# Performance work log

Measured on AMD Instinct MI355X. Metric: run time of the kernel, lower is better.

The kernel has to match this reference:

```python
import math
import jax, jax.numpy as jnp
import numpy as np

EMB = 1024
NHEADS = 16
CTX = 2048
LN_EPS = 1e-5


def new_gelu(x):
    c = math.sqrt(2.0 / math.pi)
    return 0.5 * x * (1.0 + jnp.tanh(c * (x + 0.044715 * x * x * x)))


def layer_norm(x, g, b):
    mu = jnp.mean(x, axis=-1, keepdims=True)
    var = jnp.mean(jnp.square(x - mu), axis=-1, keepdims=True)
    return (x - mu) * jax.lax.rsqrt(var + LN_EPS) * g + b


def setup_inputs() -> dict:
    key = jax.random.key(0)
    ks = jax.random.split(key, 12)
    s = 0.02
    return {
        "x": jax.random.normal(ks[0], (2, 2048, EMB), dtype=jnp.float32),
        "ln1_g": jnp.ones((EMB,), jnp.float32),
        "ln1_b": jnp.zeros((EMB,), jnp.float32),
        "W_attn": jax.random.normal(ks[1], (EMB, 3 * EMB), jnp.float32) * s,
        "b_attn": jnp.zeros((3 * EMB,), jnp.float32),
        "W_attn_proj": jax.random.normal(ks[2], (EMB, EMB), jnp.float32) * s,
        "b_attn_proj": jnp.zeros((EMB,), jnp.float32),
        "ln2_g": jnp.ones((EMB,), jnp.float32),
        "ln2_b": jnp.zeros((EMB,), jnp.float32),
        "W_fc": jax.random.normal(ks[3], (EMB, 4 * EMB), jnp.float32) * s,
        "b_fc": jnp.zeros((4 * EMB,), jnp.float32),
        "W_mlp_proj": jax.random.normal(ks[4], (4 * EMB, EMB), jnp.float32) * s,
        "b_mlp_proj": jnp.zeros((EMB,), jnp.float32),
    }


def reference(x, ln1_g, ln1_b, W_attn, b_attn, W_attn_proj, b_attn_proj,
              ln2_g, ln2_b, W_fc, b_fc, W_mlp_proj, b_mlp_proj):
    B, S, E = x.shape
    hd = E // NHEADS

    # x = ln_1(x)
    x = layer_norm(x, ln1_g, ln1_b)

    # attention on normalized x
    qkv = x @ W_attn + b_attn                      # [B,S,3E]
    q, k, v = jnp.split(qkv, 3, axis=-1)
    q = q.reshape(B, S, NHEADS, hd).transpose(0, 2, 1, 3)  # [B,H,S,hd]
    k = k.reshape(B, S, NHEADS, hd).transpose(0, 2, 1, 3)
    v = v.reshape(B, S, NHEADS, hd).transpose(0, 2, 1, 3)

    attn = jnp.einsum("bhqd,bhkd->bhqk", q, k) * (1.0 / math.sqrt(hd))
    causal = jnp.tril(jnp.ones((S, S), dtype=bool))
    attn = jnp.where(causal[None, None], attn, -jnp.inf)
    attn = jax.nn.softmax(attn, axis=-1)
    out = jnp.einsum("bhqk,bhkd->bhqd", attn, v)   # [B,H,S,hd]
    out = out.transpose(0, 2, 1, 3).reshape(B, S, E)
    out = out @ W_attn_proj + b_attn_proj

    x = x + out

    # x = ln_2(x)
    x = layer_norm(x, ln2_g, ln2_b)

    # MLP on normalized x
    h = new_gelu(x @ W_fc + b_fc)
    h = h @ W_mlp_proj + b_mlp_proj
    return x + h
```

## Files before the change

kernel.cpp:

```cpp
#include <hip/hip_runtime.h>
#include <cstdint>

typedef __attribute__((ext_vector_type(8))) short bf16x8;
typedef __attribute__((ext_vector_type(4))) float f32x4;
typedef __attribute__((ext_vector_type(16))) float f32x16;
typedef __attribute__((ext_vector_type(4))) unsigned short u16x4;
typedef __attribute__((ext_vector_type(4))) unsigned int u32x4;
typedef unsigned short u16;

#define LOG2E 1.44269504088896340736f

__device__ __forceinline__ u16 f2bf(float f) {
  unsigned u = __builtin_bit_cast(unsigned, f);
  u += 0x7FFFu + ((u >> 16) & 1u);
  return (u16)(u >> 16);
}
__device__ __forceinline__ float bf2f(u16 h) {
  return __builtin_bit_cast(float, ((unsigned)h) << 16);
}

#define GLOAD_LDS16(g, l)                                                              \
  __builtin_amdgcn_global_load_lds((const __attribute__((address_space(1))) void*)(g), \
                                   (__attribute__((address_space(3))) void*)(l), 16, 0, 0)

__global__ __launch_bounds__(256) void k_transpose_all(
    const float* __restrict__ W0, u16* __restrict__ T0,
    const float* __restrict__ W1, u16* __restrict__ T1,
    const float* __restrict__ W2, u16* __restrict__ T2,
    const float* __restrict__ W3, u16* __restrict__ T3) {
  __shared__ float tile[32][33];
  int b = blockIdx.x;
  const float* W;
  u16* Wt;
  int K, N, nx;
  if (b < 3072)        { W = W0; Wt = T0; K = 1024; N = 3072; nx = 96; }
  else if (b < 4096)   { b -= 3072; W = W1; Wt = T1; K = 1024; N = 1024; nx = 32; }
  else if (b < 8192)   { b -= 4096; W = W2; Wt = T2; K = 1024; N = 4096; nx = 128; }
  else                 { b -= 8192; W = W3; Wt = T3; K = 4096; N = 1024; nx = 32; }
  const int n0 = (b % nx) * 32, k0 = (b / nx) * 32;
  const int tid = threadIdx.x;
  const int tx = tid & 31, ty = tid >> 5;
#pragma unroll
  for (int i = 0; i < 32; i += 8)
    tile[ty + i][tx] = W[(size_t)(k0 + ty + i) * N + n0 + tx];
  __syncthreads();
#pragma unroll
  for (int i = 0; i < 32; i += 8)
    Wt[(size_t)(n0 + ty + i) * K + k0 + tx] = f2bf(tile[tx][ty + i]);
}

template <bool INF32>
__global__ __launch_bounds__(256) void k_layernorm(
    const void* __restrict__ xin, const float* __restrict__ g,
    const float* __restrict__ b, u16* __restrict__ y) {
  const int row = blockIdx.x, tid = threadIdx.x;
  float v0, v1, v2, v3;
  if (INF32) {
    const float4 v = ((const float4*)((const float*)xin + (size_t)row * 1024))[tid];
    v0 = v.x; v1 = v.y; v2 = v.z; v3 = v.w;
  } else {
    const u16x4 v = ((const u16x4*)((const u16*)xin + (size_t)row * 1024))[tid];
    v0 = bf2f(v[0]); v1 = bf2f(v[1]); v2 = bf2f(v[2]); v3 = bf2f(v[3]);
  }
  float s = v0 + v1 + v2 + v3;
#pragma unroll
  for (int m = 1; m < 64; m <<= 1) s += __shfl_xor(s, m);
  __shared__ float ps[8];
  if ((tid & 63) == 0) ps[tid >> 6] = s;
  __syncthreads();
  const float mean = (ps[0] + ps[1] + ps[2] + ps[3]) * (1.0f / 1024.0f);
  const float d0 = v0 - mean, d1 = v1 - mean, d2 = v2 - mean, d3 = v3 - mean;
  float s2 = d0 * d0 + d1 * d1 + d2 * d2 + d3 * d3;
#pragma unroll
  for (int m = 1; m < 64; m <<= 1) s2 += __shfl_xor(s2, m);
  if ((tid & 63) == 0) ps[4 + (tid >> 6)] = s2;
  __syncthreads();
  const float var = (ps[4] + ps[5] + ps[6] + ps[7]) * (1.0f / 1024.0f);
  const float rstd = rsqrtf(var + 1e-5f);
  const float4 gv = ((const float4*)g)[tid];
  const float4 bv = ((const float4*)b)[tid];
  u16x4 o;
  o[0] = f2bf(d0 * rstd * gv.x + bv.x);
  o[1] = f2bf(d1 * rstd * gv.y + bv.y);
  o[2] = f2bf(d2 * rstd * gv.z + bv.z);
  o[3] = f2bf(d3 * rstd * gv.w + bv.w);
  *(u16x4*)(y + (size_t)row * 1024 + tid * 4) = o;
}

__device__ __forceinline__ float gelu_f(float x) {
  const float u = 0.7978845608028654f * (x + 0.044715f * x * x * x);
  const float e = exp2f(u * 2.8853900817779268f);
  const float t = 1.0f - 2.0f / (e + 1.0f);
  return 0.5f * x * (1.0f + t);
}

template <int EPI, int BN>
__global__ __launch_bounds__(256, 4) void k_gemm_bt(
    const u16* __restrict__ A, const u16* __restrict__ Bt,
    const float* __restrict__ bias, const u16* __restrict__ resid,
    void* __restrict__ out, u16* __restrict__ vt, int M, int N, int K, int nbx) {
  constexpr int BM = 128;
  constexpr int LOOPB = (BM * 64 + BN * 64) * 2;
  constexpr int STP = BN + 8;
  constexpr int EPIB = (EPI == 1) ? 64 * 68 * 4 : BM * STP * 2;
  constexpr int SMB = LOOPB > EPIB ? LOOPB : EPIB;
  __shared__ char smem[SMB];
  u16* As = (u16*)smem;
  u16* Bs = (u16*)(smem + BM * 64 * 2);
  const int tid = threadIdx.x;
  const int wg = ((blockIdx.x & 7) * (gridDim.x >> 3)) + (blockIdx.x >> 3);
  const int bx = wg % nbx, by = wg / nbx;
  const int rowBase = by * BM, colBase = bx * BN;
  const int w = tid >> 6, l = tid & 63;
  const int wm = (BN == 128) ? (w >> 1) : w;
  const int wn = (BN == 128) ? (w & 1) : 0;
  constexpr int MR = (BN == 128) ? 4 : 2;
  constexpr int WROWS = (BN == 128) ? 64 : 32;
  const int lrow = l & 15, lg = l >> 4;
  const int srow = tid >> 3, sslot = tid & 7;

  const f32x4 fz = {0.f, 0.f, 0.f, 0.f};
  f32x4 acc[MR][4];
#pragma unroll
  for (int m = 0; m < MR; m++)
#pragma unroll
    for (int n = 0; n < 4; n++) acc[m][n] = fz;

  const int NT = K >> 6;
  for (int kt = 0; kt < NT; ++kt) {
#pragma unroll
    for (int i = 0; i < BM / 32; i++) {
      const int r = srow + 32 * i;
      const int gs = sslot ^ (r & 7);
      GLOAD_LDS16(A + (size_t)(rowBase + r) * K + kt * 64 + gs * 8,
                  (char*)As + i * 4096 + tid * 16);
    }
#pragma unroll
    for (int i = 0; i < BN / 32; i++) {
      const int r = srow + 32 * i;
      const int gs = sslot ^ (r & 7);
      GLOAD_LDS16(Bt + (size_t)(colBase + r) * K + kt * 64 + gs * 8,
                  (char*)Bs + i * 4096 + tid * 16);
    }
    __syncthreads();
#pragma unroll
    for (int kc = 0; kc < 2; kc++) {
      bf16x8 av[MR], bv[4];
#pragma unroll
      for (int m = 0; m < MR; m++) {
        const int r = wm * WROWS + m * 16 + lrow;
        const int sl = (kc * 4 + lg) ^ (r & 7);
        av[m] = *(const bf16x8*)((const char*)As + r * 128 + sl * 16);
      }
#pragma unroll
      for (int n = 0; n < 4; n++) {
        const int r = wn * 64 + n * 16 + lrow;
        const int sl = (kc * 4 + lg) ^ (r & 7);
        bv[n] = *(const bf16x8*)((const char*)Bs + r * 128 + sl * 16);
      }
#pragma unroll
      for (int m = 0; m < MR; m++)
#pragma unroll
        for (int n = 0; n < 4; n++)
          acc[m][n] = __builtin_amdgcn_mfma_f32_16x16x32_bf16(av[m], bv[n], acc[m][n], 0, 0, 0);
    }
    __syncthreads();
  }

  if (EPI == 1) {
    float* stgf = (float*)smem;
#pragma unroll
    for (int m = 0; m < MR; m++) {
      if (m) __syncthreads();
#pragma unroll
      for (int n = 0; n < 4; n++) {
        const int col = n * 16 + lrow;
        const float bval = bias[colBase + col];
        const int pr0 = wm * 16 + lg * 4;
#pragma unroll
        for (int r = 0; r < 4; r++) stgf[(pr0 + r) * 68 + col] = acc[m][n][r] + bval;
      }
      __syncthreads();
#pragma unroll
      for (int i = 0; i < 4; i++) {
        const int c = i * 256 + tid;
        const int pr = c >> 4, ch = c & 15;
        float4 d = *(float4*)(stgf + pr * 68 + ch * 4);
        const int grow = rowBase + ((pr >> 4) << 5) + m * 16 + (pr & 15);
        const size_t gidx = (size_t)grow * N + colBase + ch * 4;
        const u16x4 rr = *(const u16x4*)(resid + gidx);
        d.x += bf2f(rr[0]); d.y += bf2f(rr[1]); d.z += bf2f(rr[2]); d.w += bf2f(rr[3]);
        *(float4*)((float*)out + gidx) = d;
      }
    }
  } else {
    u16* stg = (u16*)smem;
    const bool vpath = (EPI == 3) && (colBase >= 2048);
#pragma unroll
    for (int n = 0; n < 4; n++) {
      const int col = wn * 64 + n * 16 + lrow;
      const float bval = bias[colBase + col];
#pragma unroll
      for (int m = 0; m < MR; m++) {
        const int lr0 = wm * WROWS + m * 16 + lg * 4;
#pragma unroll
        for (int r = 0; r < 4; r++) {
          float v = acc[m][n][r] + bval;
          if (EPI == 2) v = gelu_f(v);
          if (vpath)
            stg[col * STP + lr0 + r] = f2bf(v);
          else
            stg[(lr0 + r) * STP + col] = f2bf(v);
        }
      }
    }
    __syncthreads();
    if (vpath) {
      const int cb = colBase - 2048;
      const int bat = rowBase >> 11, tok0 = rowBase & 2047;
#pragma unroll
      for (int i = 0; i < 8; i++) {
        const int c = i * 256 + tid;
        const int cr = c >> 4, ch = c & 15;
        const u32x4 d = *(u32x4*)(stg + cr * STP + ch * 8);
        const int hh = (cb + cr) >> 6, dd = (cb + cr) & 63;
        *(u32x4*)(vt + ((size_t)(bat * 16 + hh) * 64 + dd) * 2048 + tok0 + ch * 8) = d;
      }
    } else {
      const int outN = (EPI == 3) ? 2048 : N;
      constexpr int CH = BN / 8;
#pragma unroll
      for (int i = 0; i < BM * CH / 256; i++) {
        const int c = i * 256 + tid;
        const int row = c / CH, ch = c % CH;
        u32x4 d = *(u32x4*)(stg + row * STP + ch * 8);
        const size_t gidx = (size_t)(rowBase + row) * outN + colBase + ch * 8;
        if (EPI == 4) {
          const u32x4 rr = *(const u32x4*)(resid + gidx);
#pragma unroll
          for (int j = 0; j < 4; j++) {
            const unsigned a = d[j], b = rr[j];
            const unsigned lo2 = (unsigned)f2bf(bf2f((u16)a) + bf2f((u16)b));
            const unsigned hi2 = (unsigned)f2bf(bf2f((u16)(a >> 16)) + bf2f((u16)(b >> 16)));
            d[j] = lo2 | (hi2 << 16);
          }
        }
        *(u32x4*)((u16*)out + gidx) = d;
      }
    }
  }
}

__global__ __launch_bounds__(256, 2) void k_attention(
    const u16* __restrict__ qk, const u16* __restrict__ VT, u16* __restrict__ out) {
  const int S = 2048, E2 = 2048;
  const int bid = blockIdx.x;
  const int qt = 15 - (bid >> 5);
  const int bh = bid & 31;
  const int bat = bh >> 4, h = bh & 15;
  const u16* base = qk + (size_t)bat * S * E2;
  const u16* kbase = base + 1024 + h * 64;
  const u16* vbase = VT + (size_t)bh * 64 * S;
  const int tid = threadIdx.x, w = tid >> 6, l = tid & 63;
  const int l31 = l & 31, lh = l >> 5;
  __shared__ u16 Ks[2][128 * 64];
  __shared__ u16 Vs[2][64 * 128];
  const int ksrow = tid >> 3;
  const int kgs = (tid & 7) ^ (ksrow & 7);
  const int vsrow = tid >> 4;
  const int vgs = (tid & 15) ^ (vsrow & 15);
  const float sc = 0.125f * LOG2E;
  const float RTHR = 8.0f / sc;

  auto STAGE = [&](int bufi, int kb) {
#pragma unroll
    for (int i = 0; i < 4; i++) {
      const int kr = ksrow + 32 * i;
      GLOAD_LDS16(kbase + (size_t)(kb + kr) * E2 + kgs * 8,
                  (char*)Ks[bufi] + i * 4096 + tid * 16);
      const int vr = vsrow + 16 * i;
      GLOAD_LDS16(vbase + (size_t)vr * S + kb + vgs * 8,
                  (char*)Vs[bufi] + i * 4096 + tid * 16);
    }
  };

  const int wq0 = qt * 128 + w * 32;
  const int qg = wq0 + l31;
  const int nkt = qt + 1;

  bf16x8 qf[4];
#pragma unroll
  for (int s = 0; s < 4; s++)
    qf[s] = *(const bf16x8*)(base + (size_t)qg * E2 + h * 64 + s * 16 + lh * 8);

  f32x16 o0, o1;
#pragma unroll
  for (int r = 0; r < 16; r++) { o0[r] = 0.f; o1[r] = 0.f; }
  float mrow = -1e30f, lsum = 0.f;

  STAGE(0, 0);
  __syncthreads();

  for (int t = 0; t < nkt; t++) {
    const int cur = t & 1;
    const int kb = t * 128;
    if (t + 1 < nkt) STAGE(cur ^ 1, kb + 128);
    const u16* Kc = Ks[cur];
    const u16* Vc = Vs[cur];

    f32x16 sv[4];
#pragma unroll
    for (int j = 0; j < 4; j++)
#pragma unroll
      for (int r = 0; r < 16; r++) sv[j][r] = 0.f;
#pragma unroll
    for (int s = 0; s < 4; s++) {
      const int sl = s * 2 + lh;
#pragma unroll
      for (int j = 0; j < 4; j++) {
        const int rk = j * 32 + l31;
        const bf16x8 kf = *(const bf16x8*)(Kc + rk * 64 + ((sl ^ (rk & 7)) * 8));
        sv[j] = __builtin_amdgcn_mfma_f32_32x32x16_bf16(kf, qf[s], sv[j], 0, 0, 0);
      }
    }

    if (t == nkt - 1) {
#pragma unroll
      for (int j = 0; j < 4; j++)
#pragma unroll
        for (int reg = 0; reg < 16; reg++) {
          const int kl = (reg & 3) + 8 * (reg >> 2) + 4 * lh;
          if (kb + j * 32 + kl > qg) sv[j][reg] = -1e30f;
        }
    }

    float tmax = sv[0][0];
#pragma unroll
    for (int j = 0; j < 4; j++)
#pragma unroll
      for (int reg = 0; reg < 16; reg++) tmax = fmaxf(tmax, sv[j][reg]);
    tmax = fmaxf(tmax, __shfl_xor(tmax, 32));

    if (!__all(tmax - mrow <= RTHR)) {
      const float mnew = fmaxf(mrow, tmax);
      const float corr = exp2f((mrow - mnew) * sc);
      lsum *= corr;
#pragma unroll
      for (int reg = 0; reg < 16; reg++) { o0[reg] *= corr; o1[reg] *= corr; }
      mrow = mnew;
    }
    const float msc = mrow * sc;

    float rsum = 0.f;
#pragma unroll
    for (int j = 0; j < 4; j++)
#pragma unroll
      for (int reg = 0; reg < 16; reg++) {
        const float p = exp2f(fmaf(sv[j][reg], sc, -msc));
        sv[j][reg] = p;
        rsum += p;
      }
    rsum += __shfl_xor(rsum, 32);
    lsum += rsum;

    const bool lo = (lh == 0);
#pragma unroll
    for (int j = 0; j < 4; j++) {
      unsigned pk[8], ex[8];
#pragma unroll
      for (int jj = 0; jj < 8; jj++) {
        asm("v_cvt_pk_bf16_f32 %0, %1, %2"
            : "=v"(pk[jj])
            : "v"(sv[j][2 * jj]), "v"(sv[j][2 * jj + 1]));
        ex[jj] = (unsigned)__shfl_xor((int)pk[jj], 32);
      }
#pragma unroll
      for (int sl2 = 0; sl2 < 2; sl2++) {
        const int ks = j * 2 + sl2;
        const int j0 = sl2 * 4;
        const unsigned b0 = lo ? pk[j0 + 0] : ex[j0 + 2];
        const unsigned b1 = lo ? pk[j0 + 1] : ex[j0 + 3];
        const unsigned b2 = lo ? ex[j0 + 0] : pk[j0 + 2];
        const unsigned b3 = lo ? ex[j0 + 1] : pk[j0 + 3];
        const u32x4 pbu = {b0, b1, b2, b3};
        const bf16x8 pb = __builtin_bit_cast(bf16x8, pbu);
        const int svl = ks * 2 + lh;
        const int r0 = l31, r1 = 32 + l31;
        const bf16x8 v0 = *(const bf16x8*)(Vc + r0 * 128 + ((svl ^ (r0 & 15)) * 8));
        const bf16x8 v1 = *(const bf16x8*)(Vc + r1 * 128 + ((svl ^ (r1 & 15)) * 8));
        o0 = __builtin_amdgcn_mfma_f32_32x32x16_bf16(v0, pb, o0, 0, 0, 0);
        o1 = __builtin_amdgcn_mfma_f32_32x32x16_bf16(v1, pb, o1, 0, 0, 0);
      }
    }
    __syncthreads();
  }

  const float inv = 1.0f / lsum;
  const size_t orow = (size_t)(bat * S + qg) * 1024 + h * 64;
#pragma unroll
  for (int g = 0; g < 4; g++) {
    u16x4 s0, s1;
#pragma unroll
    for (int r = 0; r < 4; r++) {
      s0[r] = f2bf(o0[4 * g + r] * inv);
      s1[r] = f2bf(o1[4 * g + r] * inv);
    }
    const int d0 = 8 * g + 4 * lh;
    *(u16x4*)(out + orow + d0) = s0;
    *(u16x4*)(out + orow + 32 + d0) = s1;
  }
}

extern "C" void kernel_launch(void* const* d_in, const int* in_sizes, int n_in,
                              void* d_out, int out_size, void* d_ws, size_t ws_size,
                              hipStream_t stream) {
  (void)in_sizes; (void)n_in; (void)out_size; (void)ws_size;
  const float* x      = (const float*)d_in[0];
  const float* ln1_g  = (const float*)d_in[1];
  const float* ln1_b  = (const float*)d_in[2];
  const float* W_attn = (const float*)d_in[3];
  const float* b_attn = (const float*)d_in[4];
  const float* W_proj = (const float*)d_in[5];
  const float* b_proj = (const float*)d_in[6];
  const float* ln2_g  = (const float*)d_in[7];
  const float* ln2_b  = (const float*)d_in[8];
  const float* W_fc   = (const float*)d_in[9];
  const float* b_fc   = (const float*)d_in[10];
  const float* W_mlp  = (const float*)d_in[11];
  const float* b_mlp  = (const float*)d_in[12];

  const int M = 4096;
  char* ws = (char*)d_ws;
  size_t off = 0;
  auto alloc = [&](size_t bytes) {
    void* p = ws + off;
    off += (bytes + 255) & ~(size_t)255;
    return p;
  };
  u16* WattnT = (u16*)alloc((size_t)3072 * 1024 * 2);
  u16* WprojT = (u16*)alloc((size_t)1024 * 1024 * 2);
  u16* WfcT   = (u16*)alloc((size_t)4096 * 1024 * 2);
  u16* WmlpT  = (u16*)alloc((size_t)1024 * 4096 * 2);
  u16* x1     = (u16*)alloc((size_t)M * 1024 * 2);
  u16* qkb    = (u16*)alloc((size_t)M * 2048 * 2);
  u16* VT     = (u16*)alloc((size_t)32 * 64 * 2048 * 2);
  u16* attno  = (u16*)alloc((size_t)M * 1024 * 2);
  u16* x2     = (u16*)alloc((size_t)M * 1024 * 2);
  u16* x3     = (u16*)alloc((size_t)M * 1024 * 2);
  u16* hbuf   = (u16*)alloc((size_t)M * 4096 * 2);

  const dim3 blk(256);
  k_transpose_all<<<dim3(12288), blk, 0, stream>>>(
      W_attn, WattnT, W_proj, WprojT, W_fc, WfcT, W_mlp, WmlpT);

  k_layernorm<true><<<M, blk, 0, stream>>>(x, ln1_g, ln1_b, x1);
  k_gemm_bt<3, 128><<<dim3(768), blk, 0, stream>>>(
      x1, WattnT, b_attn, nullptr, qkb, VT, M, 3072, 1024, 24);
  k_attention<<<dim3(512), blk, 0, stream>>>(qkb, VT, attno);
  k_gemm_bt<4, 64><<<dim3(512), blk, 0, stream>>>(
      attno, WprojT, b_proj, x1, x2, nullptr, M, 1024, 1024, 16);
  k_layernorm<false><<<M, blk, 0, stream>>>(x2, ln2_g, ln2_b, x3);
  k_gemm_bt<2, 128><<<dim3(1024), blk, 0, stream>>>(
      x3, WfcT, b_fc, nullptr, hbuf, nullptr, M, 4096, 1024, 32);
  k_gemm_bt<1, 64><<<dim3(512), blk, 0, stream>>>(
      hbuf, WmlpT, b_mlp, x3, d_out, nullptr, M, 1024, 4096, 16);
}
```

Measured before the change: 235.8 us.

## Split long causal attention query tiles across two key ranges and combine

Query tiles 8-15, which carry the longest causal key ranges, are each split into two blocks that cover halves of the key range. Each half writes unnormalized fp32 partial outputs plus its row max and sum to workspace, and a new combine kernel merges them with log-sum-exp weights. The grid grows from 512 to 768 blocks, which evens out per-block work and cuts the long tail on the causal triangle. The cost is an extra kernel launch and fp32 partial-output traffic.

```diff
diff --git a/kernel.cpp b/kernel.cpp
--- a/kernel.cpp
+++ b/kernel.cpp
@@ -252,11 +252,20 @@
 }
 
 __global__ __launch_bounds__(256, 2) void k_attention(
-    const u16* __restrict__ qk, const u16* __restrict__ VT, u16* __restrict__ out) {
+    const u16* __restrict__ qk, const u16* __restrict__ VT, u16* __restrict__ out,
+    float* __restrict__ Op0, float* __restrict__ Op1,
+    float2* __restrict__ ml0, float2* __restrict__ ml1) {
   const int S = 2048, E2 = 2048;
   const int bid = blockIdx.x;
-  const int qt = 15 - (bid >> 5);
-  const int bh = bid & 31;
+  const int u = bid >> 5, bh = bid & 31;
+  int qt, piece;
+  if (u < 8)       { qt = 15 - u;      piece = 0; }
+  else if (u < 16) { qt = 15 - (u - 8); piece = 1; }
+  else             { qt = 23 - u;      piece = 2; }
+  const int nkt = qt + 1;
+  const int h0 = (nkt + 1) >> 1;
+  const int t0 = (piece == 1) ? h0 : 0;
+  const int t1 = (piece == 0) ? h0 : nkt;
   const int bat = bh >> 4, h = bh & 15;
   const u16* base = qk + (size_t)bat * S * E2;
   const u16* kbase = base + 1024 + h * 64;
@@ -286,7 +295,6 @@
 
   const int wq0 = qt * 128 + w * 32;
   const int qg = wq0 + l31;
-  const int nkt = qt + 1;
 
   bf16x8 qf[4];
 #pragma unroll
@@ -298,13 +306,13 @@
   for (int r = 0; r < 16; r++) { o0[r] = 0.f; o1[r] = 0.f; }
   float mrow = -1e30f, lsum = 0.f;
 
-  STAGE(0, 0);
+  STAGE(0, t0 * 128);
   __syncthreads();
 
-  for (int t = 0; t < nkt; t++) {
-    const int cur = t & 1;
+  for (int t = t0; t < t1; t++) {
+    const int cur = (t - t0) & 1;
     const int kb = t * 128;
-    if (t + 1 < nkt) STAGE(cur ^ 1, kb + 128);
+    if (t + 1 < t1) STAGE(cur ^ 1, kb + 128);
     const u16* Kc = Ks[cur];
     const u16* Vc = Vs[cur];
 
@@ -395,20 +403,57 @@
     __syncthreads();
   }
 
-  const float inv = 1.0f / lsum;
-  const size_t orow = (size_t)(bat * S + qg) * 1024 + h * 64;
-#pragma unroll
-  for (int g = 0; g < 4; g++) {
-    u16x4 s0, s1;
-#pragma unroll
-    for (int r = 0; r < 4; r++) {
-      s0[r] = f2bf(o0[4 * g + r] * inv);
-      s1[r] = f2bf(o1[4 * g + r] * inv);
-    }
-    const int d0 = 8 * g + 4 * lh;
-    *(u16x4*)(out + orow + d0) = s0;
-    *(u16x4*)(out + orow + 32 + d0) = s1;
+  if (piece == 2) {
+    const float inv = 1.0f / lsum;
+    const size_t orow = (size_t)(bat * S + qg) * 1024 + h * 64;
+#pragma unroll
+    for (int g = 0; g < 4; g++) {
+      u16x4 s0, s1;
+#pragma unroll
+      for (int r = 0; r < 4; r++) {
+        s0[r] = f2bf(o0[4 * g + r] * inv);
+        s1[r] = f2bf(o1[4 * g + r] * inv);
+      }
+      const int d0 = 8 * g + 4 * lh;
+      *(u16x4*)(out + orow + d0) = s0;
+      *(u16x4*)(out + orow + 32 + d0) = s1;
+    }
+  } else {
+    float* Op = piece ? Op1 : Op0;
+    float2* mlp = piece ? ml1 : ml0;
+    const size_t rix = (size_t)bh * 1024 + (qg - 1024);
+    const size_t rbase = rix * 64;
+#pragma unroll
+    for (int g = 0; g < 4; g++) {
+      const int d0 = 8 * g + 4 * lh;
+      float4 a, b;
+      a.x = o0[4 * g]; a.y = o0[4 * g + 1]; a.z = o0[4 * g + 2]; a.w = o0[4 * g + 3];
+      b.x = o1[4 * g]; b.y = o1[4 * g + 1]; b.z = o1[4 * g + 2]; b.w = o1[4 * g + 3];
+      *(float4*)(Op + rbase + d0) = a;
+      *(float4*)(Op + rbase + 32 + d0) = b;
+    }
+    if (lh == 0) mlp[rix] = make_float2(mrow, lsum);
   }
+}
+
+__global__ __launch_bounds__(256) void k_attn_combine(
+    const float* __restrict__ Op0, const float* __restrict__ Op1,
+    const float2* __restrict__ ml0, const float2* __restrict__ ml1,
+    u16* __restrict__ out) {
+  const float sc = 0.125f * LOG2E;
+  const int idx = blockIdx.x * 256 + threadIdx.x;
+  const int d = idx & 63;
+  const int row = idx >> 6;
+  const int bh = row >> 10;
+  const int qg = 1024 + (row & 1023);
+  const int bat = bh >> 4, h = bh & 15;
+  const float2 a = ml0[row], b = ml1[row];
+  const float mf = fmaxf(a.x, b.x);
+  const float w1 = exp2f((a.x - mf) * sc);
+  const float w2 = exp2f((b.x - mf) * sc);
+  const float linv = 1.0f / (a.y * w1 + b.y * w2);
+  const float o = (Op0[(size_t)row * 64 + d] * w1 + Op1[(size_t)row * 64 + d] * w2) * linv;
+  out[(size_t)(bat * 2048 + qg) * 1024 + h * 64 + d] = f2bf(o);
 }
 
 extern "C" void kernel_launch(void* const* d_in, const int* in_sizes, int n_in,
@@ -448,6 +493,10 @@
   u16* x2     = (u16*)alloc((size_t)M * 1024 * 2);
   u16* x3     = (u16*)alloc((size_t)M * 1024 * 2);
   u16* hbuf   = (u16*)alloc((size_t)M * 4096 * 2);
+  float*  Op0 = (float*)alloc((size_t)32 * 1024 * 64 * 4);
+  float*  Op1 = (float*)alloc((size_t)32 * 1024 * 64 * 4);
+  float2* ml0 = (float2*)alloc((size_t)32 * 1024 * 8);
+  float2* ml1 = (float2*)alloc((size_t)32 * 1024 * 8);
 
   const dim3 blk(256);
   k_transpose_all<<<dim3(12288), blk, 0, stream>>>(
@@ -456,7 +505,8 @@
   k_layernorm<true><<<M, blk, 0, stream>>>(x, ln1_g, ln1_b, x1);
   k_gemm_bt<3, 128><<<dim3(768), blk, 0, stream>>>(
       x1, WattnT, b_attn, nullptr, qkb, VT, M, 3072, 1024, 24);
-  k_attention<<<dim3(512), blk, 0, stream>>>(qkb, VT, attno);
+  k_attention<<<dim3(768), blk, 0, stream>>>(qkb, VT, attno, Op0, Op1, ml0, ml1);
+  k_attn_combine<<<dim3(32 * 1024 * 64 / 256), blk, 0, stream>>>(Op0, Op1, ml0, ml1, attno);
   k_gemm_bt<4, 64><<<dim3(512), blk, 0, stream>>>(
       attno, WprojT, b_proj, x1, x2, nullptr, M, 1024, 1024, 16);
   k_layernorm<false><<<M, blk, 0, stream>>>(x2, ln2_g, ln2_b, x3);
```

Measured after the change: 239.0 us. Within noise of the previous version (+1.4%).
